# Kernel optimization log

Hardware: AMD Instinct MI355X
Metric: run time of the kernel (lower is better)

The kernel has to match this reference:

```python
import jax, jax.numpy as jnp
import numpy as np

MARGIN = 0.3
EPS = 1e-6  # torch pairwise_distance eps (added to the difference before norm)


def _sample_triplets(labels, B):
    """Vectorized equivalent of the per-row nonzero()+randint() mining loop.

    pos_idx[i] ~ Uniform{j : labels[j] == labels[i]}   (always non-empty: i itself)
    neg_idx[i] ~ Uniform{j : labels[j] != labels[i]}, fallback Uniform[0,B) if empty.
    Uniform-noise argmax over the masked set == uniform random choice.
    """
    key = jax.random.key(42)
    k1, k2, k3 = jax.random.split(key, 3)
    eq = labels[:, None] == labels[None, :]              # [B, B]
    pos_idx = jnp.argmax(jnp.where(eq, jax.random.uniform(k1, (B, B)), -1.0), axis=1)
    neg_scores = jnp.where(~eq, jax.random.uniform(k2, (B, B)), -1.0)
    has_neg = jnp.any(~eq, axis=1)
    neg_idx = jnp.where(has_neg,
                        jnp.argmax(neg_scores, axis=1),
                        jax.random.randint(k3, (B,), 0, B))
    return pos_idx, neg_idx


def _pdist(X, A, D):
    """out[i, j] = || A[j] - X[i] + EPS ||_2  (torch pairwise_distance semantics),
    computed via gram matrices instead of a [B,B,D] intermediate:
    ||a - x + eps||^2 = ||a||^2 + ||x||^2 - 2 a.x + 2*eps*(sum a - sum x) + D*eps^2.
    """
    sq = (jnp.sum(A * A, axis=1)[None, :]
          + jnp.sum(X * X, axis=1)[:, None]
          - 2.0 * (X @ A.T)
          + 2.0 * EPS * (jnp.sum(A, axis=1)[None, :] - jnp.sum(X, axis=1)[:, None])
          + D * EPS * EPS)
    return jnp.sqrt(jnp.maximum(sq, 1e-12))


def setup_inputs() -> dict:
    key = jax.random.key(0)
    kf, kl = jax.random.split(key)
    B, D, NUM_IDS = 4096, 1024, 512
    features = jax.random.normal(kf, (B, D), dtype=jnp.float32)
    labels = jax.random.randint(kl, (B,), 0, NUM_IDS, dtype=jnp.int32)
    return {"features": features, "labels": labels}


def reference(features, labels):
    B, D = features.shape
    pos_idx, neg_idx = _sample_triplets(labels, B)
    P = features[pos_idx]   # positives, [B, D]
    N = features[neg_idx]   # negatives, [B, D]
    # Original torch code stacks positives/negatives as [B,1,D] vs anchors [B,D],
    # so TripletMarginLoss broadcasts to ALL-PAIRS [B,B] distances:
    # dap[i, j] = ||anchor_j - positive_i + eps||, same for dan.
    dap = _pdist(P, features, D)  # [B, B]
    dan = _pdist(N, features, D)  # [B, B]
    return jnp.mean(jax.nn.relu(dap - dan + MARGIN))
```

## Files before the change

### kernel.cpp

```cpp
#include <hip/hip_runtime.h>
#include <stdint.h>

#define BSZ 4096
#define DIM 1024
#define EPSV 1e-6f
#define MARGINV 0.3f
#define SROWS 4
#define LROWS 4
#define GEMM_BLOCKS 528
#define SAMPLE_BLOCKS (BSZ / SROWS)
#define PREP_BLOCKS (BSZ / 4)
#define LOSS_BLOCKS (BSZ / LROWS)

#define TF_ROT(x0, x1, r) { x0 += x1; x1 = ((x1 << r) | (x1 >> (32 - r))); x1 ^= x0; }

__host__ __device__ __forceinline__ void threefry2x32(uint32_t k0, uint32_t k1,
                                                      uint32_t c0, uint32_t c1,
                                                      uint32_t& o0, uint32_t& o1) {
  uint32_t ks2 = k0 ^ k1 ^ 0x1BD11BDAu;
  uint32_t x0 = c0 + k0;
  uint32_t x1 = c1 + k1;
  TF_ROT(x0, x1, 13) TF_ROT(x0, x1, 15) TF_ROT(x0, x1, 26) TF_ROT(x0, x1, 6)
  x0 += k1;  x1 += ks2 + 1u;
  TF_ROT(x0, x1, 17) TF_ROT(x0, x1, 29) TF_ROT(x0, x1, 16) TF_ROT(x0, x1, 24)
  x0 += ks2; x1 += k0 + 2u;
  TF_ROT(x0, x1, 13) TF_ROT(x0, x1, 15) TF_ROT(x0, x1, 26) TF_ROT(x0, x1, 6)
  x0 += k0;  x1 += k1 + 3u;
  TF_ROT(x0, x1, 17) TF_ROT(x0, x1, 29) TF_ROT(x0, x1, 16) TF_ROT(x0, x1, 24)
  x0 += k1;  x1 += ks2 + 4u;
  TF_ROT(x0, x1, 13) TF_ROT(x0, x1, 15) TF_ROT(x0, x1, 26) TF_ROT(x0, x1, 6)
  x0 += ks2; x1 += k0 + 5u;
  o0 = x0; o1 = x1;
}

#define TFR2(r) { xa0 += xa1; xb0 += xb1; \
                  xa1 = ((xa1 << r) | (xa1 >> (32 - r))) ^ xa0; \
                  xb1 = ((xb1 << r) | (xb1 >> (32 - r))) ^ xb0; }

__device__ __forceinline__ void threefry_x2(uint32_t k0, uint32_t k1,
                                            uint32_t ca, uint32_t cb,
                                            uint32_t& oa, uint32_t& ob) {
  const uint32_t ks2 = k0 ^ k1 ^ 0x1BD11BDAu;
  uint32_t xa0 = k0, xa1 = ca + k1;
  uint32_t xb0 = k0, xb1 = cb + k1;
  TFR2(13) TFR2(15) TFR2(26) TFR2(6)
  xa0 += k1;  xa1 += ks2 + 1u;  xb0 += k1;  xb1 += ks2 + 1u;
  TFR2(17) TFR2(29) TFR2(16) TFR2(24)
  xa0 += ks2; xa1 += k0 + 2u;   xb0 += ks2; xb1 += k0 + 2u;
  TFR2(13) TFR2(15) TFR2(26) TFR2(6)
  xa0 += k0;  xa1 += k1 + 3u;   xb0 += k0;  xb1 += k1 + 3u;
  TFR2(17) TFR2(29) TFR2(16) TFR2(24)
  xa0 += k1;  xa1 += ks2 + 4u;  xb0 += k1;  xb1 += ks2 + 4u;
  TFR2(13) TFR2(15) TFR2(26) TFR2(6)
  xa0 += ks2; xa1 += k0 + 5u;   xb0 += ks2; xb1 += k0 + 5u;
  oa = xa0 ^ xa1;
  ob = xb0 ^ xb1;
}

__device__ __forceinline__ uint16_t f2bf(float f) {
  uint32_t u = __float_as_uint(f);
  u += 0x7FFFu + ((u >> 16) & 1u);
  return (uint16_t)(u >> 16);
}

__global__ __launch_bounds__(256, 8) void prep_sample_kernel(
    const float* __restrict__ F, uint8_t* __restrict__ Fq,
    float* __restrict__ norm2, float* __restrict__ sums, float* __restrict__ nv,
    const int* __restrict__ labels, int* __restrict__ pos_idx, int* __restrict__ neg_idx,
    uint32_t p0, uint32_t p1, uint32_t n0, uint32_t n1) {
  __shared__ int plist[SROWS * 64];
  __shared__ int pcnt[SROWS];
  __shared__ unsigned long long swp[SROWS];
  __shared__ unsigned long long swn[SROWS];
  const int t = threadIdx.x;

  if (blockIdx.x >= SAMPLE_BLOCKS) {
    const int w = t >> 6, l = t & 63;
    const int r = (blockIdx.x - SAMPLE_BLOCKS) * 4 + w;
    const float4* src = (const float4*)(F + (size_t)r * DIM);
    uint32_t* dst = (uint32_t*)(Fq + (size_t)r * DIM);
    float s = 0.f, q = 0.f;
#pragma unroll
    for (int c = 0; c < 4; ++c) {
      float4 v = src[c * 64 + l];
      s += (v.x + v.y) + (v.z + v.w);
      q += v.x * v.x + v.y * v.y + v.z * v.z + v.w * v.w;
      int wd = 0;
      wd = __builtin_amdgcn_cvt_pk_fp8_f32(v.x, v.y, wd, false);
      wd = __builtin_amdgcn_cvt_pk_fp8_f32(v.z, v.w, wd, true);
      dst[c * 64 + l] = (uint32_t)wd;
    }
    for (int off = 32; off; off >>= 1) { s += __shfl_xor(s, off); q += __shfl_xor(q, off); }
    if (l == 0) {
      norm2[r] = q; sums[r] = s;
      nv[r] = q + 2.0f * EPSV * s;
    }
    return;
  }

  const int i0 = blockIdx.x * SROWS;
  if (t < SROWS) { pcnt[t] = 0; swp[t] = 0ull; swn[t] = 0ull; }
  int lj[16];
#pragma unroll
  for (int c = 0; c < 16; ++c) lj[c] = labels[c * 256 + t];
  __syncthreads();
  const int lane = t & 63;
#pragma unroll 1
  for (int r = 0; r < SROWS; ++r) {
    const int li = labels[i0 + r];
    const uint32_t base = (uint32_t)(i0 + r) * (uint32_t)BSZ + (uint32_t)t;
    uint32_t bestn = 0u;
#pragma unroll
    for (int c = 0; c < 16; c += 2) {
      uint32_t bitsA, bitsB;
      threefry_x2(n0, n1, base + (uint32_t)(c * 256), base + (uint32_t)((c + 1) * 256),
                  bitsA, bitsB);
      const uint32_t packA = ((bitsA >> 5) & 0xFFFFFFF0u) | (uint32_t)(15 - c);
      const uint32_t packB = ((bitsB >> 5) & 0xFFFFFFF0u) | (uint32_t)(14 - c);
      const uint32_t vA = (lj[c] == li) ? 0u : packA;
      const uint32_t vB = (lj[c + 1] == li) ? 0u : packB;
      const uint32_t mab = vA > vB ? vA : vB;
      bestn = bestn > mab ? bestn : mab;
    }
    unsigned long long keyn = 0ull;
    if (bestn) {
      const int c = 15 - (int)(bestn & 15u);
      const int j = c * 256 + t;
      keyn = ((unsigned long long)(bestn >> 4) << 32) | (uint32_t)(~j);
    }
    for (int off = 32; off; off >>= 1) {
      unsigned long long o = __shfl_xor(keyn, off);
      if (o > keyn) keyn = o;
    }
    if (lane == 0) atomicMax(&swn[r], keyn);
#pragma unroll
    for (int c = 0; c < 16; ++c) {
      if (lj[c] == li) {
        int sl = atomicAdd(&pcnt[r], 1);
        if (sl < 64) plist[r * 64 + sl] = c * 256 + t;
      }
    }
  }
  __syncthreads();
  const int w = t >> 6;
  {
    const int cnt = pcnt[w] < 64 ? pcnt[w] : 64;
    if (lane < cnt) {
      const int j = plist[w * 64 + lane];
      uint32_t y0, y1;
      threefry2x32(p0, p1, 0u, (uint32_t)(i0 + w) * (uint32_t)BSZ + (uint32_t)j, y0, y1);
      const unsigned long long key =
          ((unsigned long long)((y0 ^ y1) >> 9) << 32) | (uint32_t)(~j);
      atomicMax(&swp[w], key);
    }
  }
  __syncthreads();
  if (t < SROWS) {
    pos_idx[i0 + t] = (int)(~(uint32_t)swp[t]);
    const unsigned long long vn = swn[t];
    neg_idx[i0 + t] = (vn == 0ull) ? 0 : (int)(~(uint32_t)vn);
  }
}

using int8v = __attribute__((ext_vector_type(8))) int;
using int4v = __attribute__((ext_vector_type(4))) int;
using f32x4 = __attribute__((ext_vector_type(4))) float;

__device__ __forceinline__ void async_load16(const void* g, void* l) {
  __builtin_amdgcn_global_load_lds((__attribute__((address_space(1))) void*)g,
                                   (__attribute__((address_space(3))) void*)l, 16, 0, 0);
}

__global__ __launch_bounds__(256, 4) void gemm_kernel(
    const uint8_t* __restrict__ Fq, uint16_t* __restrict__ Gb) {
  __shared__ __align__(16) uint8_t lA[128 * 128];
  __shared__ __align__(16) uint8_t lB[128 * 128];
  const int t = threadIdx.x;

  const int p = blockIdx.x;
  int by = (int)((sqrtf(8.0f * (float)p + 1.0f) - 1.0f) * 0.5f);
  if ((by + 1) * (by + 2) / 2 <= p) ++by;
  if (by * (by + 1) / 2 > p) --by;
  const int bx = p - by * (by + 1) / 2;

  const int l = t & 63;
  const int w = t >> 6;
  const int wm = (w >> 1) * 64;
  const int wn = (w & 1) * 64;
  const int bm = bx * 128;
  const int bn = by * 128;

  f32x4 acc[4][4] = {};

  const int srow = t >> 3;
  const int scol = (((t & 7) ^ ((t >> 3) & 7)) << 4);
  const uint8_t* gA0 = Fq + (size_t)(bm + srow) * DIM + scol;
  const uint8_t* gB0 = Fq + (size_t)(bn + srow) * DIM + scol;

  const int fr = l & 15;
  const int c0 = (l >> 4) * 2;
  int offA[4][2], offB[4][2];
#pragma unroll
  for (int tm = 0; tm < 4; ++tm) {
    const int fra = wm + tm * 16 + fr, sw = fra & 7;
    offA[tm][0] = fra * 128 + ((c0 ^ sw) << 4);
    offA[tm][1] = fra * 128 + (((c0 + 1) ^ sw) << 4);
    const int frb = wn + tm * 16 + fr, sb = frb & 7;
    offB[tm][0] = frb * 128 + ((c0 ^ sb) << 4);
    offB[tm][1] = frb * 128 + (((c0 + 1) ^ sb) << 4);
  }

  for (int it = 0; it < 8; ++it) {
    const int k0 = it * 128;
    __syncthreads();
#pragma unroll
    for (int ld = 0; ld < 4; ++ld) {
      async_load16(gA0 + (size_t)ld * 32 * DIM + k0, (char*)lA + (ld * 256 + t) * 16);
      async_load16(gB0 + (size_t)ld * 32 * DIM + k0, (char*)lB + (ld * 256 + t) * 16);
    }
    __syncthreads();
    int8v av[4], bv[4];
#pragma unroll
    for (int tm = 0; tm < 4; ++tm) {
      int4v alo = *(const int4v*)&lA[offA[tm][0]];
      int4v ahi = *(const int4v*)&lA[offA[tm][1]];
      av[tm] = __builtin_shufflevector(alo, ahi, 0, 1, 2, 3, 4, 5, 6, 7);
      int4v blo = *(const int4v*)&lB[offB[tm][0]];
      int4v bhi = *(const int4v*)&lB[offB[tm][1]];
      bv[tm] = __builtin_shufflevector(blo, bhi, 0, 1, 2, 3, 4, 5, 6, 7);
    }
#pragma unroll
    for (int tm = 0; tm < 4; ++tm)
#pragma unroll
      for (int tn = 0; tn < 4; ++tn)
        acc[tm][tn] = __builtin_amdgcn_mfma_scale_f32_16x16x128_f8f6f4(
            av[tm], bv[tn], acc[tm][tn],
            0, 0,
            0, 0x7F7F7F7F,
            0, 0x7F7F7F7F);
  }
  const int cr = (l >> 4) * 4;
  const int cc = l & 15;
#pragma unroll
  for (int tm = 0; tm < 4; ++tm)
#pragma unroll
    for (int tn = 0; tn < 4; ++tn) {
      const int row0 = bm + wm + tm * 16 + cr;
      const int col  = bn + wn + tn * 16 + cc;
      ushort h0 = f2bf(acc[tm][tn][0]), h1 = f2bf(acc[tm][tn][1]);
      ushort h2 = f2bf(acc[tm][tn][2]), h3 = f2bf(acc[tm][tn][3]);
      Gb[(size_t)(row0 + 0) * BSZ + col] = h0;
      Gb[(size_t)(row0 + 1) * BSZ + col] = h1;
      Gb[(size_t)(row0 + 2) * BSZ + col] = h2;
      Gb[(size_t)(row0 + 3) * BSZ + col] = h3;
      ushort4 v = make_ushort4(h0, h1, h2, h3);
      *(ushort4*)&Gb[(size_t)col * BSZ + row0] = v;
    }
}

__device__ __forceinline__ float bfl(uint32_t w) { return __uint_as_float(w << 16); }
__device__ __forceinline__ float bfh(uint32_t w) { return __uint_as_float(w & 0xFFFF0000u); }

__global__ __launch_bounds__(256) void loss_kernel(const uint16_t* __restrict__ Gb,
                                                   const float* __restrict__ norm2,
                                                   const float* __restrict__ sums,
                                                   const float* __restrict__ nv,
                                                   const int* __restrict__ pos_idx,
                                                   const int* __restrict__ neg_idx,
                                                   float* __restrict__ partial) {
  const int i0 = blockIdx.x * LROWS, t = threadIdx.x;
  const float deps2 = (float)DIM * EPSV * EPSV;
  const float4* N4 = (const float4*)nv;
  float4 njv[4];
#pragma unroll
  for (int k = 0; k < 4; ++k) njv[k] = N4[t * 4 + k];
  __shared__ float ps[4];
  const int w = t >> 6, lane = t & 63;
#pragma unroll 1
  for (int r = 0; r < LROWS; ++r) {
    const int i = i0 + r;
    const int a = pos_idx[i], b = neg_idx[i];
    const float ca = norm2[a] - 2.0f * EPSV * sums[a] + deps2;
    const float cb = norm2[b] - 2.0f * EPSV * sums[b] + deps2;
    const uint4* Ga = (const uint4*)(Gb + (size_t)a * BSZ);
    const uint4* Gn = (const uint4*)(Gb + (size_t)b * BSZ);
    uint4 ga[2], gn[2];
    ga[0] = Ga[t * 2]; ga[1] = Ga[t * 2 + 1];
    gn[0] = Gn[t * 2]; gn[1] = Gn[t * 2 + 1];
    float s = 0.f;
#pragma unroll
    for (int h = 0; h < 2; ++h) {
      const uint4 gau = ga[h], gnu = gn[h];
      float gav[8] = {bfl(gau.x), bfh(gau.x), bfl(gau.y), bfh(gau.y),
                      bfl(gau.z), bfh(gau.z), bfl(gau.w), bfh(gau.w)};
      float gnv[8] = {bfl(gnu.x), bfh(gnu.x), bfl(gnu.y), bfh(gnu.y),
                      bfl(gnu.z), bfh(gnu.z), bfl(gnu.w), bfh(gnu.w)};
      const float4 na = njv[h * 2], nb = njv[h * 2 + 1];
      float nj[8] = {na.x, na.y, na.z, na.w, nb.x, nb.y, nb.z, nb.w};
#pragma unroll
      for (int e = 0; e < 8; ++e) {
        const float dap = sqrtf(fmaxf(fmaf(-2.f, gav[e], nj[e] + ca), 1e-12f));
        const float dan = sqrtf(fmaxf(fmaf(-2.f, gnv[e], nj[e] + cb), 1e-12f));
        s += fmaxf(dap - dan + MARGINV, 0.f);
      }
    }
    for (int off = 32; off; off >>= 1) s += __shfl_xor(s, off);
    if (lane == 0) ps[w] = s;
    __syncthreads();
    if (t == 0) partial[i] = (ps[0] + ps[1]) + (ps[2] + ps[3]);
    __syncthreads();
  }
}

__global__ __launch_bounds__(256) void finalize_kernel(const float* __restrict__ partial,
                                                       float* __restrict__ out) {
  const int t = threadIdx.x;
  const float4* P4 = (const float4*)partial;
  float s = 0.f;
#pragma unroll
  for (int k = 0; k < 4; ++k) {
    float4 v = P4[k * 256 + t];
    s += (v.x + v.y) + (v.z + v.w);
  }
  for (int off = 32; off; off >>= 1) s += __shfl_xor(s, off);
  __shared__ float ps[4];
  const int w = t >> 6, lane = t & 63;
  if (lane == 0) ps[w] = s;
  __syncthreads();
  if (t == 0)
    out[0] = ((ps[0] + ps[1]) + (ps[2] + ps[3])) * (1.0f / ((float)BSZ * (float)BSZ));
}

extern "C" void kernel_launch(void* const* d_in, const int* in_sizes, int n_in,
                              void* d_out, int out_size, void* d_ws, size_t ws_size,
                              hipStream_t stream) {
  const float* feat = (const float*)d_in[0];
  const int* labels = (const int*)d_in[1];
  float* out = (float*)d_out;

  char* ws = (char*)d_ws;
  uint16_t* Gb     = (uint16_t*)ws;
  uint8_t* Fq      = (uint8_t*)(ws + (size_t)33554432);
  float* norm2     = (float*)(ws + (size_t)37748736);
  float* sums      = (float*)(ws + (size_t)37748736 + 16384);
  float* nv        = (float*)(ws + (size_t)37748736 + 32768);
  int* pos_idx     = (int*)  (ws + (size_t)37748736 + 49152);
  int* neg_idx     = (int*)  (ws + (size_t)37748736 + 65536);
  float* partial   = (float*)(ws + (size_t)37748736 + 81920);

  uint32_t k1a, k1b, k2a, k2b;
  threefry2x32(0u, 42u, 0u, 0u, k1a, k1b);
  threefry2x32(0u, 42u, 0u, 1u, k2a, k2b);

  prep_sample_kernel<<<dim3(SAMPLE_BLOCKS + PREP_BLOCKS), dim3(256), 0, stream>>>(
      feat, Fq, norm2, sums, nv, labels, pos_idx, neg_idx, k1a, k1b, k2a, k2b);
  gemm_kernel<<<dim3(GEMM_BLOCKS), dim3(256), 0, stream>>>(Fq, Gb);
  loss_kernel<<<dim3(LOSS_BLOCKS), dim3(256), 0, stream>>>(Gb, norm2, sums, nv,
                                                           pos_idx, neg_idx, partial);
  finalize_kernel<<<dim3(1), dim3(256), 0, stream>>>(partial, out);
}
```

Baseline: 150.9 us.

## Double-buffer GEMM LDS tiles and use one row per loss block

New measurement: 139.8 us. 1.08x faster.

```diff
diff --git a/kernel.cpp b/kernel.cpp
--- a/kernel.cpp
+++ b/kernel.cpp
@@ -6,11 +6,9 @@
 #define EPSV 1e-6f
 #define MARGINV 0.3f
 #define SROWS 4
-#define LROWS 4
 #define GEMM_BLOCKS 528
 #define SAMPLE_BLOCKS (BSZ / SROWS)
 #define PREP_BLOCKS (BSZ / 4)
-#define LOSS_BLOCKS (BSZ / LROWS)
 
 #define TF_ROT(x0, x1, r) { x0 += x1; x1 = ((x1 << r) | (x1 >> (32 - r))); x1 ^= x0; }
 
@@ -171,10 +169,10 @@
                                    (__attribute__((address_space(3))) void*)l, 16, 0, 0);
 }
 
-__global__ __launch_bounds__(256, 4) void gemm_kernel(
+__global__ __launch_bounds__(256, 2) void gemm_kernel(
     const uint8_t* __restrict__ Fq, uint16_t* __restrict__ Gb) {
-  __shared__ __align__(16) uint8_t lA[128 * 128];
-  __shared__ __align__(16) uint8_t lB[128 * 128];
+  __shared__ __align__(16) uint8_t lA[2][128 * 128];
+  __shared__ __align__(16) uint8_t lB[2][128 * 128];
   const int t = threadIdx.x;
 
   const int p = blockIdx.x;
@@ -210,23 +208,33 @@
     offB[tm][1] = frb * 128 + (((c0 + 1) ^ sb) << 4);
   }
 
+#pragma unroll
+  for (int ld = 0; ld < 4; ++ld) {
+    async_load16(gA0 + (size_t)ld * 32 * DIM, (char*)lA[0] + (ld * 256 + t) * 16);
+    async_load16(gB0 + (size_t)ld * 32 * DIM, (char*)lB[0] + (ld * 256 + t) * 16);
+  }
+  __syncthreads();
+
   for (int it = 0; it < 8; ++it) {
-    const int k0 = it * 128;
-    __syncthreads();
-#pragma unroll
-    for (int ld = 0; ld < 4; ++ld) {
-      async_load16(gA0 + (size_t)ld * 32 * DIM + k0, (char*)lA + (ld * 256 + t) * 16);
-      async_load16(gB0 + (size_t)ld * 32 * DIM + k0, (char*)lB + (ld * 256 + t) * 16);
-    }
-    __syncthreads();
+    const int cur = it & 1;
+    if (it < 7) {
+      const int k1 = (it + 1) * 128;
+#pragma unroll
+      for (int ld = 0; ld < 4; ++ld) {
+        async_load16(gA0 + (size_t)ld * 32 * DIM + k1,
+                     (char*)lA[cur ^ 1] + (ld * 256 + t) * 16);
+        async_load16(gB0 + (size_t)ld * 32 * DIM + k1,
+                     (char*)lB[cur ^ 1] + (ld * 256 + t) * 16);
+      }
+    }
     int8v av[4], bv[4];
 #pragma unroll
     for (int tm = 0; tm < 4; ++tm) {
-      int4v alo = *(const int4v*)&lA[offA[tm][0]];
-      int4v ahi = *(const int4v*)&lA[offA[tm][1]];
+      int4v alo = *(const int4v*)&lA[cur][offA[tm][0]];
+      int4v ahi = *(const int4v*)&lA[cur][offA[tm][1]];
       av[tm] = __builtin_shufflevector(alo, ahi, 0, 1, 2, 3, 4, 5, 6, 7);
-      int4v blo = *(const int4v*)&lB[offB[tm][0]];
-      int4v bhi = *(const int4v*)&lB[offB[tm][1]];
+      int4v blo = *(const int4v*)&lB[cur][offB[tm][0]];
+      int4v bhi = *(const int4v*)&lB[cur][offB[tm][1]];
       bv[tm] = __builtin_shufflevector(blo, bhi, 0, 1, 2, 3, 4, 5, 6, 7);
     }
 #pragma unroll
@@ -238,6 +246,7 @@
             0, 0,
             0, 0x7F7F7F7F,
             0, 0x7F7F7F7F);
+    __syncthreads();
   }
   const int cr = (l >> 4) * 4;
   const int cc = l & 15;
@@ -268,48 +277,43 @@
                                                    const int* __restrict__ pos_idx,
                                                    const int* __restrict__ neg_idx,
                                                    float* __restrict__ partial) {
-  const int i0 = blockIdx.x * LROWS, t = threadIdx.x;
+  const int i = blockIdx.x, t = threadIdx.x;
+  const int a = pos_idx[i], b = neg_idx[i];
   const float deps2 = (float)DIM * EPSV * EPSV;
+  const float ca = norm2[a] - 2.0f * EPSV * sums[a] + deps2;
+  const float cb = norm2[b] - 2.0f * EPSV * sums[b] + deps2;
+  const uint4* Ga = (const uint4*)(Gb + (size_t)a * BSZ);
+  const uint4* Gn = (const uint4*)(Gb + (size_t)b * BSZ);
   const float4* N4 = (const float4*)nv;
+  uint4 ga[2], gn[2];
   float4 njv[4];
+  ga[0] = Ga[t * 2]; ga[1] = Ga[t * 2 + 1];
+  gn[0] = Gn[t * 2]; gn[1] = Gn[t * 2 + 1];
 #pragma unroll
   for (int k = 0; k < 4; ++k) njv[k] = N4[t * 4 + k];
+  float s = 0.f;
+#pragma unroll
+  for (int h = 0; h < 2; ++h) {
+    const uint4 gau = ga[h], gnu = gn[h];
+    float gav[8] = {bfl(gau.x), bfh(gau.x), bfl(gau.y), bfh(gau.y),
+                    bfl(gau.z), bfh(gau.z), bfl(gau.w), bfh(gau.w)};
+    float gnv[8] = {bfl(gnu.x), bfh(gnu.x), bfl(gnu.y), bfh(gnu.y),
+                    bfl(gnu.z), bfh(gnu.z), bfl(gnu.w), bfh(gnu.w)};
+    const float4 na = njv[h * 2], nb = njv[h * 2 + 1];
+    float nj[8] = {na.x, na.y, na.z, na.w, nb.x, nb.y, nb.z, nb.w};
+#pragma unroll
+    for (int e = 0; e < 8; ++e) {
+      const float dap = sqrtf(fmaxf(fmaf(-2.f, gav[e], nj[e] + ca), 1e-12f));
+      const float dan = sqrtf(fmaxf(fmaf(-2.f, gnv[e], nj[e] + cb), 1e-12f));
+      s += fmaxf(dap - dan + MARGINV, 0.f);
+    }
+  }
+  for (int off = 32; off; off >>= 1) s += __shfl_xor(s, off);
   __shared__ float ps[4];
   const int w = t >> 6, lane = t & 63;
-#pragma unroll 1
-  for (int r = 0; r < LROWS; ++r) {
-    const int i = i0 + r;
-    const int a = pos_idx[i], b = neg_idx[i];
-    const float ca = norm2[a] - 2.0f * EPSV * sums[a] + deps2;
-    const float cb = norm2[b] - 2.0f * EPSV * sums[b] + deps2;
-    const uint4* Ga = (const uint4*)(Gb + (size_t)a * BSZ);
-    const uint4* Gn = (const uint4*)(Gb + (size_t)b * BSZ);
-    uint4 ga[2], gn[2];
-    ga[0] = Ga[t * 2]; ga[1] = Ga[t * 2 + 1];
-    gn[0] = Gn[t * 2]; gn[1] = Gn[t * 2 + 1];
-    float s = 0.f;
-#pragma unroll
-    for (int h = 0; h < 2; ++h) {
-      const uint4 gau = ga[h], gnu = gn[h];
-      float gav[8] = {bfl(gau.x), bfh(gau.x), bfl(gau.y), bfh(gau.y),
-                      bfl(gau.z), bfh(gau.z), bfl(gau.w), bfh(gau.w)};
-      float gnv[8] = {bfl(gnu.x), bfh(gnu.x), bfl(gnu.y), bfh(gnu.y),
-                      bfl(gnu.z), bfh(gnu.z), bfl(gnu.w), bfh(gnu.w)};
-      const float4 na = njv[h * 2], nb = njv[h * 2 + 1];
-      float nj[8] = {na.x, na.y, na.z, na.w, nb.x, nb.y, nb.z, nb.w};
-#pragma unroll
-      for (int e = 0; e < 8; ++e) {
-        const float dap = sqrtf(fmaxf(fmaf(-2.f, gav[e], nj[e] + ca), 1e-12f));
-        const float dan = sqrtf(fmaxf(fmaf(-2.f, gnv[e], nj[e] + cb), 1e-12f));
-        s += fmaxf(dap - dan + MARGINV, 0.f);
-      }
-    }
-    for (int off = 32; off; off >>= 1) s += __shfl_xor(s, off);
-    if (lane == 0) ps[w] = s;
-    __syncthreads();
-    if (t == 0) partial[i] = (ps[0] + ps[1]) + (ps[2] + ps[3]);
-    __syncthreads();
-  }
+  if (lane == 0) ps[w] = s;
+  __syncthreads();
+  if (t == 0) partial[i] = (ps[0] + ps[1]) + (ps[2] + ps[3]);
 }
 
 __global__ __launch_bounds__(256) void finalize_kernel(const float* __restrict__ partial,
@@ -355,7 +359,7 @@
   prep_sample_kernel<<<dim3(SAMPLE_BLOCKS + PREP_BLOCKS), dim3(256), 0, stream>>>(
       feat, Fq, norm2, sums, nv, labels, pos_idx, neg_idx, k1a, k1b, k2a, k2b);
   gemm_kernel<<<dim3(GEMM_BLOCKS), dim3(256), 0, stream>>>(Fq, Gb);
-  loss_kernel<<<dim3(LOSS_BLOCKS), dim3(256), 0, stream>>>(Gb, norm2, sums, nv,
-                                                           pos_idx, neg_idx, partial);
+  loss_kernel<<<dim3(BSZ), dim3(256), 0, stream>>>(Gb, norm2, sums, nv, pos_idx,
+                                                   neg_idx, partial);
   finalize_kernel<<<dim3(1), dim3(256), 0, stream>>>(partial, out);
 }
```
